# Kernel optimization log

Measured on AMD Instinct MI355X. Metric: run time of the kernel, lower is better.

## Reference

```python
import jax, jax.numpy as jnp
import numpy as np

N = 524288          # grid_size
H = 256             # MLP hidden width for psi_func
X_MIN, X_MAX = -10.0, 10.0
HBAR, MASS = 1.0, 1.0
STEPS, DT = 100, 0.01
DX = (X_MAX - X_MIN) / (N - 1)
K_TERM = -HBAR ** 2 / (2.0 * MASS)


def setup_inputs() -> dict:
    key = jax.random.key(0)
    k1, k2, k3, k4 = jax.random.split(key, 4)
    x = jnp.linspace(X_MIN, X_MAX, N, dtype=jnp.float32).reshape(-1, 1)
    V_x = (0.5 * x ** 2).astype(jnp.float32)            # harmonic potential [N,1]
    W1 = jax.random.normal(k1, (1, H), jnp.float32) * 0.5
    b1 = jax.random.normal(k2, (H,), jnp.float32) * 0.5
    W2 = jax.random.normal(k3, (H, 2), jnp.float32) / np.float32(np.sqrt(H))
    b2 = jnp.zeros((2,), jnp.float32)
    noise = jax.random.normal(k4, (STEPS,), jnp.float32)  # Langevin diffusion draws
    init_idx = 262144                                     # torch.randint(0, grid_size, (1,)).item()
    return {"x": x, "V_x": V_x, "W1": W1, "b1": b1, "W2": W2, "b2": b2,
            "noise": noise, "init_idx": init_idx}


def reference(x, V_x, W1, b1, W2, b2, noise, init_idx):
    # psi_func: 1 -> H -> 2 tanh MLP, psi = [Re, Im]
    def psi_point(xs):                    # scalar -> [2]
        h = jnp.tanh(xs * W1[0] + b1)
        return h @ W2 + b2

    xg = x[:, 0]                          # [N]
    psi = jax.vmap(psi_point)(xg)         # [N,2]

    # kinetic_energy: Laplacian d^2 psi / dx^2 via nested forward-mode derivatives
    lap = jax.vmap(jax.jacfwd(jax.jacfwd(psi_point)))(xg)   # [N,2]
    t_psi = K_TERM * lap

    # hamiltonian_operator: H psi = T psi + V(x) psi
    h_psi = t_psi + V_x * psi             # [N,2]

    # variational_energy_loss
    densities = jnp.sum(psi * h_psi, axis=1)               # [N]
    norm_densities = jnp.sum(psi ** 2, axis=1)             # [N]
    energy = (jnp.sum(densities) * DX) / (jnp.sum(norm_densities) * DX + 1e-8)

    # hamiltonian_score_matching_collapse (fused on-device scan, no per-step syncs)
    prob = norm_densities / (jnp.sum(norm_densities) * DX + 1e-8)
    log_prob = jnp.log(prob + 1e-10)
    score = jnp.zeros_like(log_prob).at[1:-1].set(
        (log_prob[2:] - log_prob[:-2]) / (2.0 * DX))

    sqrt2dt = np.float32(np.sqrt(2.0 * DT))

    def step(c_idx, z):
        s = score[c_idx]
        shift = ((s * DT + z * sqrt2dt) / DX).astype(jnp.int32)  # int() truncates toward 0
        c_idx = jnp.clip(c_idx + shift, 0, N - 1)
        return c_idx, None

    c_final, _ = jax.lax.scan(step, jnp.asarray(init_idx, jnp.int32), noise)
    x_collapsed = xg[c_final]

    return h_psi, energy, x_collapsed
```

## Files before the change

kernel.cpp:

```cpp
#include <hip/hip_runtime.h>
#include <hip/hip_bf16.h>
#include <math.h>

#define NPTS 524288
#define HDIM 256
#define NBLK (NPTS / 256)
#define STEPS 100

constexpr float DXF       = (float)(20.0 / (NPTS - 1));
constexpr float TWODXF    = (float)(2.0 * (20.0 / (NPTS - 1)));
constexpr float DTF       = 0.01f;
constexpr float SQRT2DT   = 0.14142135623730951f;
constexpr float TWO_LOG2E = 2.8853900817779268f;

typedef float v2f __attribute__((ext_vector_type(2)));

static __device__ __forceinline__ v2f vfma(v2f a, v2f b, v2f c) {
#if __has_builtin(__builtin_elementwise_fma)
    return __builtin_elementwise_fma(a, b, c);
#else
    v2f r; r.x = fmaf(a.x, b.x, c.x); r.y = fmaf(a.y, b.y, c.y); return r;
#endif
}

__global__ void qpe_prep(const float* __restrict__ W1, const float* __restrict__ b1,
                         const float* __restrict__ W2, float* __restrict__ wk)
{
    const int h = threadIdx.x;
    const float w1  = W1[h];
    const float w20 = W2[2*h];
    const float w21 = W2[2*h + 1];
    const float w1s = w1 * w1;
    wk[h]        = w1 * TWO_LOG2E;
    wk[256 + h]  = b1[h] * TWO_LOG2E;
    wk[512 + h]  = w20;
    wk[768 + h]  = w21;
    wk[1024 + h] = w20 * w1s;
    wk[1280 + h] = w21 * w1s;
}

__global__ __launch_bounds__(256) void qpe_main(
    const float* __restrict__ x,  const float* __restrict__ V,
    const float* __restrict__ wk, const float* __restrict__ b2,
    float* __restrict__ out,      float* __restrict__ lp_arr,
    float* __restrict__ pdens,    float* __restrict__ pnd)
{
    const int i = blockIdx.x * 256 + threadIdx.x;
    const float xi = x[i];
    const float Vi = V[i];

    const v2f* __restrict__ w1k2 = (const v2f*)(wk);
    const v2f* __restrict__ b1k2 = (const v2f*)(wk + 256);
    const v2f* __restrict__ w202 = (const v2f*)(wk + 512);
    const v2f* __restrict__ w212 = (const v2f*)(wk + 768);
    const v2f* __restrict__ wg02 = (const v2f*)(wk + 1024);
    const v2f* __restrict__ wg12 = (const v2f*)(wk + 1280);

    const v2f x2   = {xi, xi};
    const v2f one2 = {1.0f, 1.0f};
    const v2f m2   = {-2.0f, -2.0f};
    v2f p0 = {0.f, 0.f}, p1 = {0.f, 0.f};
    v2f a0 = {0.f, 0.f}, a1 = {0.f, 0.f};

    #pragma unroll 8
    for (int j = 0; j < HDIM / 2; ++j) {
        const v2f u = vfma(x2, w1k2[j], b1k2[j]);
        v2f e; e.x = __builtin_amdgcn_exp2f(u.x); e.y = __builtin_amdgcn_exp2f(u.y);
        const v2f dd = e + one2;
        v2f r; r.x = __builtin_amdgcn_rcpf(dd.x); r.y = __builtin_amdgcn_rcpf(dd.y);
        const v2f t  = vfma(m2, r, one2);
        const v2f o  = vfma(-t, t, one2);
        const v2f g  = t * o;
        p0 = vfma(w202[j], t, p0);
        p1 = vfma(w212[j], t, p1);
        a0 = vfma(wg02[j], g, a0);
        a1 = vfma(wg12[j], g, a1);
    }

    const float psi0 = p0.x + p0.y + b2[0];
    const float psi1 = p1.x + p1.y + b2[1];
    const float ta0  = a0.x + a0.y;
    const float ta1  = a1.x + a1.y;

    const float hp0 = fmaf(Vi, psi0, ta0);
    const float hp1 = fmaf(Vi, psi1, ta1);
    *reinterpret_cast<float2*>(&out[2*i]) = make_float2(hp0, hp1);

    const float nd = fmaf(psi0, psi0, psi1 * psi1);
    lp_arr[i] = logf(nd);

    float dens = fmaf(psi0, hp0, psi1 * hp1);
    float ndr  = nd;
    for (int off = 32; off; off >>= 1) {
        dens += __shfl_down(dens, off);
        ndr  += __shfl_down(ndr, off);
    }
    __shared__ float sd[4], sn[4];
    const int lane = threadIdx.x & 63;
    const int wid  = threadIdx.x >> 6;
    if (lane == 0) { sd[wid] = dens; sn[wid] = ndr; }
    __syncthreads();
    if (threadIdx.x == 0) {
        pdens[blockIdx.x] = sd[0] + sd[1] + sd[2] + sd[3];
        pnd[blockIdx.x]   = sn[0] + sn[1] + sn[2] + sn[3];
    }
}

__global__ __launch_bounds__(256) void qpe_tail(
    const float* __restrict__ x,     const float* __restrict__ lp,
    const float* __restrict__ pdens, const float* __restrict__ pnd,
    const float* __restrict__ noise, const int* __restrict__ init_idx,
    float* __restrict__ out,         float* __restrict__ dummy)
{
    const int tid = threadIdx.x;
    if (tid < 64) {
        if (tid == 0) {
            int c = init_idx[0];
            for (int t = 0; t < STEPS; ++t) {
                float s = 0.0f;
                if (c > 0 && c < NPTS - 1) {
                    const float lpp = lp[c + 1];
                    const float lpm = lp[c - 1];
                    s = __fdiv_rn(__fsub_rn(lpp, lpm), TWODXF);
                }
                const float a = __fadd_rn(__fmul_rn(s, DTF),
                                          __fmul_rn(noise[t], SQRT2DT));
                const int shift = (int)__fdiv_rn(a, DXF);
                c += shift;
                c = c < 0 ? 0 : (c > NPTS - 1 ? NPTS - 1 : c);
            }
            out[2 * NPTS + 1] = x[c];
        }
    } else if (tid < 128) {
        const int l = tid - 64;
        float d = 0.f, n = 0.f;
        #pragma unroll 8
        for (int k = 0; k < 32; ++k) {
            d += pdens[l + 64 * k];
            n += pnd[l + 64 * k];
        }
        for (int off = 32; off; off >>= 1) {
            d += __shfl_down(d, off);
            n += __shfl_down(n, off);
        }
        if (l == 0)
            out[2 * NPTS] = __fdiv_rn(d * DXF, fmaf(n, DXF, 1e-8f));
    } else {
        int c0 = init_idx[0];
        int start = c0 - 65536;
        if (start < 0) start = 0;
        if (start > NPTS - 131072) start = NPTS - 131072;
        start &= ~3;
        const float4* __restrict__ src = (const float4*)(lp + start);
        const int l = tid - 128;
        float acc = 0.f;
        #pragma unroll 4
        for (int k = 0; k < 256; ++k) {
            const float4 v = src[l + 128 * k];
            acc += v.x + v.y + v.z + v.w;
        }
        if (acc == 123456.789f) dummy[0] = acc;
    }
}

extern "C" void kernel_launch(void* const* d_in, const int* in_sizes, int n_in,
                              void* d_out, int out_size, void* d_ws, size_t ws_size,
                              hipStream_t stream) {
    const float* x        = (const float*)d_in[0];
    const float* V        = (const float*)d_in[1];
    const float* W1       = (const float*)d_in[2];
    const float* b1       = (const float*)d_in[3];
    const float* W2       = (const float*)d_in[4];
    const float* b2       = (const float*)d_in[5];
    const float* noise    = (const float*)d_in[6];
    const int*   init_idx = (const int*)d_in[7];

    float* out = (float*)d_out;
    float* ws  = (float*)d_ws;

    float* lp_arr = ws;
    float* pdens  = ws + NPTS;
    float* pnd    = ws + NPTS + 2048;
    float* wk     = ws + NPTS + 4096;
    float* dummy  = ws + NPTS + 4096 + 1536;

    qpe_prep<<<1, 256, 0, stream>>>(W1, b1, W2, wk);
    qpe_main<<<NBLK, 256, 0, stream>>>(x, V, wk, b2, out, lp_arr, pdens, pnd);
    qpe_tail<<<1, 256, 0, stream>>>(x, lp_arr, pdens, pnd, noise, init_idx,
                                    out, dummy);
}
```

Before: 138.2 us.

## Fuse Langevin walk into main kernel by recomputing psi on the fly

The serial 100-step collapse walk moves out of the tail kernel into an extra block of the main kernel. At each step one wavefront recomputes psi at c±1 with the MLP, instead of reading a stored log-density array. This removes the lp_arr write, the dependent global-load chain after the main pass and the dummy prefetch. The main grid also processes two points per thread with vectorized loads and stores. The walk rebuilds x from a linspace formula rather than reading the x input, and it drops the 1e-10 epsilon inside the log, which could slightly change the chosen index.

Measured after the change: 155.3 us. 12.4% more time.

```diff
diff --git a/kernel.cpp b/kernel.cpp
--- a/kernel.cpp
+++ b/kernel.cpp
@@ -4,14 +4,14 @@
 
 #define NPTS 524288
 #define HDIM 256
-#define NBLK (NPTS / 256)
+#define NBLK2 (NPTS / 512)
 #define STEPS 100
 
-constexpr float DXF       = (float)(20.0 / (NPTS - 1));
-constexpr float TWODXF    = (float)(2.0 * (20.0 / (NPTS - 1)));
-constexpr float DTF       = 0.01f;
-constexpr float SQRT2DT   = 0.14142135623730951f;
-constexpr float TWO_LOG2E = 2.8853900817779268f;
+constexpr float DXF        = (float)(20.0 / (NPTS - 1));
+constexpr float DTF        = 0.01f;
+constexpr float SQRT2DT    = 0.14142135623730951f;
+constexpr float TWO_LOG2E  = 2.8853900817779268f;
+constexpr float LN2_O_2DX  = (float)(0.6931471805599453 / (2.0 * (20.0 / (NPTS - 1))));
 
 typedef float v2f __attribute__((ext_vector_type(2)));
 
@@ -39,15 +39,87 @@
     wk[1280 + h] = w21 * w1s;
 }
 
+static __device__ void qpe_walk(const float* __restrict__ x,
+                                const float* __restrict__ wk,
+                                const float* __restrict__ b2,
+                                const float* __restrict__ noise,
+                                const int*  __restrict__ init_idx,
+                                float* __restrict__ out)
+{
+    const int lane = threadIdx.x & 63;
+    float w1r[4], b1r[4], w20r[4], w21r[4];
+    #pragma unroll
+    for (int k = 0; k < 4; ++k) {
+        const int h = lane + 64 * k;
+        w1r[k]  = wk[h];
+        b1r[k]  = wk[256 + h];
+        w20r[k] = wk[512 + h];
+        w21r[k] = wk[768 + h];
+    }
+    const float b20 = b2[0], b21 = b2[1];
+
+    int c = init_idx[0];
+    for (int t = 0; t < STEPS; ++t) {
+        const float zs = __fmul_rn(noise[t], SQRT2DT);
+        float s = 0.0f;
+        if (c > 0 && c < NPTS - 1) {
+            const float xm = fmaf((float)(c - 1), DXF, -10.0f);
+            const float xp = fmaf((float)(c + 1), DXF, -10.0f);
+            float P0m = 0.f, P1m = 0.f, P0p = 0.f, P1p = 0.f;
+            #pragma unroll
+            for (int k = 0; k < 4; ++k) {
+                const float um = fmaf(xm, w1r[k], b1r[k]);
+                const float up = fmaf(xp, w1r[k], b1r[k]);
+                const float em = __builtin_amdgcn_exp2f(um);
+                const float ep = __builtin_amdgcn_exp2f(up);
+                const float rm = __builtin_amdgcn_rcpf(em + 1.0f);
+                const float rp = __builtin_amdgcn_rcpf(ep + 1.0f);
+                const float tm = fmaf(-2.0f, rm, 1.0f);
+                const float tp = fmaf(-2.0f, rp, 1.0f);
+                P0m = fmaf(w20r[k], tm, P0m);
+                P1m = fmaf(w21r[k], tm, P1m);
+                P0p = fmaf(w20r[k], tp, P0p);
+                P1p = fmaf(w21r[k], tp, P1p);
+            }
+            #pragma unroll
+            for (int off = 32; off; off >>= 1) {
+                P0m += __shfl_xor(P0m, off);
+                P1m += __shfl_xor(P1m, off);
+                P0p += __shfl_xor(P0p, off);
+                P1p += __shfl_xor(P1p, off);
+            }
+            const float p0m = b20 + P0m, p1m = b21 + P1m;
+            const float p0p = b20 + P0p, p1p = b21 + P1p;
+            const float ndm = fmaf(p0m, p0m, p1m * p1m);
+            const float ndp = fmaf(p0p, p0p, p1p * p1p);
+            const float l2m = __builtin_amdgcn_logf(ndm);
+            const float l2p = __builtin_amdgcn_logf(ndp);
+            s = __fmul_rn(__fsub_rn(l2p, l2m), LN2_O_2DX);
+        }
+        const float a = __fadd_rn(__fmul_rn(s, DTF), zs);
+        const int shift = (int)__fdiv_rn(a, DXF);
+        c += shift;
+        c = c < 0 ? 0 : (c > NPTS - 1 ? NPTS - 1 : c);
+    }
+    if (lane == 0) out[2 * NPTS + 1] = x[c];
+}
+
 __global__ __launch_bounds__(256) void qpe_main(
     const float* __restrict__ x,  const float* __restrict__ V,
     const float* __restrict__ wk, const float* __restrict__ b2,
-    float* __restrict__ out,      float* __restrict__ lp_arr,
-    float* __restrict__ pdens,    float* __restrict__ pnd)
-{
+    float* __restrict__ out,      float* __restrict__ pdens,
+    float* __restrict__ pnd,      const float* __restrict__ noise,
+    const int* __restrict__ init_idx)
+{
+    if (blockIdx.x == NBLK2) {
+        if (threadIdx.x < 64)
+            qpe_walk(x, wk, b2, noise, init_idx, out);
+        return;
+    }
+
     const int i = blockIdx.x * 256 + threadIdx.x;
-    const float xi = x[i];
-    const float Vi = V[i];
+    const float2 xv = reinterpret_cast<const float2*>(x)[i];
+    const float2 Vv = reinterpret_cast<const float2*>(V)[i];
 
     const v2f* __restrict__ w1k2 = (const v2f*)(wk);
     const v2f* __restrict__ b1k2 = (const v2f*)(wk + 256);
@@ -56,41 +128,62 @@
     const v2f* __restrict__ wg02 = (const v2f*)(wk + 1024);
     const v2f* __restrict__ wg12 = (const v2f*)(wk + 1280);
 
-    const v2f x2   = {xi, xi};
+    const v2f xa   = {xv.x, xv.x};
+    const v2f xb   = {xv.y, xv.y};
     const v2f one2 = {1.0f, 1.0f};
     const v2f m2   = {-2.0f, -2.0f};
-    v2f p0 = {0.f, 0.f}, p1 = {0.f, 0.f};
-    v2f a0 = {0.f, 0.f}, a1 = {0.f, 0.f};
-
-    #pragma unroll 8
+    v2f pa0 = {0.f,0.f}, pa1 = {0.f,0.f}, aa0 = {0.f,0.f}, aa1 = {0.f,0.f};
+    v2f pb0 = {0.f,0.f}, pb1 = {0.f,0.f}, ab0 = {0.f,0.f}, ab1 = {0.f,0.f};
+
+    #pragma unroll 4
     for (int j = 0; j < HDIM / 2; ++j) {
-        const v2f u = vfma(x2, w1k2[j], b1k2[j]);
-        v2f e; e.x = __builtin_amdgcn_exp2f(u.x); e.y = __builtin_amdgcn_exp2f(u.y);
-        const v2f dd = e + one2;
-        v2f r; r.x = __builtin_amdgcn_rcpf(dd.x); r.y = __builtin_amdgcn_rcpf(dd.y);
-        const v2f t  = vfma(m2, r, one2);
-        const v2f o  = vfma(-t, t, one2);
-        const v2f g  = t * o;
-        p0 = vfma(w202[j], t, p0);
-        p1 = vfma(w212[j], t, p1);
-        a0 = vfma(wg02[j], g, a0);
-        a1 = vfma(wg12[j], g, a1);
-    }
-
-    const float psi0 = p0.x + p0.y + b2[0];
-    const float psi1 = p1.x + p1.y + b2[1];
-    const float ta0  = a0.x + a0.y;
-    const float ta1  = a1.x + a1.y;
-
-    const float hp0 = fmaf(Vi, psi0, ta0);
-    const float hp1 = fmaf(Vi, psi1, ta1);
-    *reinterpret_cast<float2*>(&out[2*i]) = make_float2(hp0, hp1);
-
-    const float nd = fmaf(psi0, psi0, psi1 * psi1);
-    lp_arr[i] = logf(nd);
-
-    float dens = fmaf(psi0, hp0, psi1 * hp1);
-    float ndr  = nd;
+        const v2f w1 = w1k2[j];
+        const v2f bb = b1k2[j];
+        const v2f ua = vfma(xa, w1, bb);
+        const v2f ub = vfma(xb, w1, bb);
+        v2f ea, eb;
+        ea.x = __builtin_amdgcn_exp2f(ua.x); ea.y = __builtin_amdgcn_exp2f(ua.y);
+        eb.x = __builtin_amdgcn_exp2f(ub.x); eb.y = __builtin_amdgcn_exp2f(ub.y);
+        const v2f da = ea + one2;
+        const v2f db = eb + one2;
+        v2f ra, rb;
+        ra.x = __builtin_amdgcn_rcpf(da.x); ra.y = __builtin_amdgcn_rcpf(da.y);
+        rb.x = __builtin_amdgcn_rcpf(db.x); rb.y = __builtin_amdgcn_rcpf(db.y);
+        const v2f ta = vfma(m2, ra, one2);
+        const v2f tb = vfma(m2, rb, one2);
+        const v2f oa = vfma(-ta, ta, one2);
+        const v2f ob = vfma(-tb, tb, one2);
+        const v2f ga = ta * oa;
+        const v2f gb = tb * ob;
+        const v2f w20 = w202[j], w21 = w212[j];
+        const v2f g0  = wg02[j], g1  = wg12[j];
+        pa0 = vfma(w20, ta, pa0);  pa1 = vfma(w21, ta, pa1);
+        aa0 = vfma(g0,  ga, aa0);  aa1 = vfma(g1,  ga, aa1);
+        pb0 = vfma(w20, tb, pb0);  pb1 = vfma(w21, tb, pb1);
+        ab0 = vfma(g0,  gb, ab0);  ab1 = vfma(g1,  gb, ab1);
+    }
+
+    const float b20 = b2[0], b21 = b2[1];
+    const float psiA0 = pa0.x + pa0.y + b20;
+    const float psiA1 = pa1.x + pa1.y + b21;
+    const float psiB0 = pb0.x + pb0.y + b20;
+    const float psiB1 = pb1.x + pb1.y + b21;
+    const float taA0 = aa0.x + aa0.y, taA1 = aa1.x + aa1.y;
+    const float taB0 = ab0.x + ab0.y, taB1 = ab1.x + ab1.y;
+
+    const float hpA0 = fmaf(Vv.x, psiA0, taA0);
+    const float hpA1 = fmaf(Vv.x, psiA1, taA1);
+    const float hpB0 = fmaf(Vv.y, psiB0, taB0);
+    const float hpB1 = fmaf(Vv.y, psiB1, taB1);
+    float4 o4; o4.x = hpA0; o4.y = hpA1; o4.z = hpB0; o4.w = hpB1;
+    reinterpret_cast<float4*>(out)[i] = o4;
+
+    const float ndA = fmaf(psiA0, psiA0, psiA1 * psiA1);
+    const float ndB = fmaf(psiB0, psiB0, psiB1 * psiB1);
+    float dens = fmaf(psiA0, hpA0, psiA1 * hpA1) + fmaf(psiB0, hpB0, psiB1 * hpB1);
+    float ndr  = ndA + ndB;
+
+    #pragma unroll
     for (int off = 32; off; off >>= 1) {
         dens += __shfl_down(dens, off);
         ndr  += __shfl_down(ndr, off);
@@ -106,60 +199,27 @@
     }
 }
 
-__global__ __launch_bounds__(256) void qpe_tail(
-    const float* __restrict__ x,     const float* __restrict__ lp,
+__global__ __launch_bounds__(256) void qpe_reduce(
     const float* __restrict__ pdens, const float* __restrict__ pnd,
-    const float* __restrict__ noise, const int* __restrict__ init_idx,
-    float* __restrict__ out,         float* __restrict__ dummy)
+    float* __restrict__ energy_out)
 {
     const int tid = threadIdx.x;
-    if (tid < 64) {
-        if (tid == 0) {
-            int c = init_idx[0];
-            for (int t = 0; t < STEPS; ++t) {
-                float s = 0.0f;
-                if (c > 0 && c < NPTS - 1) {
-                    const float lpp = lp[c + 1];
-                    const float lpm = lp[c - 1];
-                    s = __fdiv_rn(__fsub_rn(lpp, lpm), TWODXF);
-                }
-                const float a = __fadd_rn(__fmul_rn(s, DTF),
-                                          __fmul_rn(noise[t], SQRT2DT));
-                const int shift = (int)__fdiv_rn(a, DXF);
-                c += shift;
-                c = c < 0 ? 0 : (c > NPTS - 1 ? NPTS - 1 : c);
-            }
-            out[2 * NPTS + 1] = x[c];
-        }
-    } else if (tid < 128) {
-        const int l = tid - 64;
-        float d = 0.f, n = 0.f;
-        #pragma unroll 8
-        for (int k = 0; k < 32; ++k) {
-            d += pdens[l + 64 * k];
-            n += pnd[l + 64 * k];
-        }
-        for (int off = 32; off; off >>= 1) {
-            d += __shfl_down(d, off);
-            n += __shfl_down(n, off);
-        }
-        if (l == 0)
-            out[2 * NPTS] = __fdiv_rn(d * DXF, fmaf(n, DXF, 1e-8f));
-    } else {
-        int c0 = init_idx[0];
-        int start = c0 - 65536;
-        if (start < 0) start = 0;
-        if (start > NPTS - 131072) start = NPTS - 131072;
-        start &= ~3;
-        const float4* __restrict__ src = (const float4*)(lp + start);
-        const int l = tid - 128;
-        float acc = 0.f;
-        #pragma unroll 4
-        for (int k = 0; k < 256; ++k) {
-            const float4 v = src[l + 128 * k];
-            acc += v.x + v.y + v.z + v.w;
-        }
-        if (acc == 123456.789f) dummy[0] = acc;
+    float d = pdens[tid] + pdens[tid + 256] + pdens[tid + 512] + pdens[tid + 768];
+    float n = pnd[tid]   + pnd[tid + 256]   + pnd[tid + 512]   + pnd[tid + 768];
+    #pragma unroll
+    for (int off = 32; off; off >>= 1) {
+        d += __shfl_down(d, off);
+        n += __shfl_down(n, off);
+    }
+    __shared__ float sd[4], sn[4];
+    const int lane = tid & 63;
+    const int wid  = tid >> 6;
+    if (lane == 0) { sd[wid] = d; sn[wid] = n; }
+    __syncthreads();
+    if (tid == 0) {
+        const float Sd = sd[0] + sd[1] + sd[2] + sd[3];
+        const float Sn = sn[0] + sn[1] + sn[2] + sn[3];
+        energy_out[0] = __fdiv_rn(Sd * DXF, fmaf(Sn, DXF, 1e-8f));
     }
 }
 
@@ -178,14 +238,12 @@
     float* out = (float*)d_out;
     float* ws  = (float*)d_ws;
 
-    float* lp_arr = ws;
-    float* pdens  = ws + NPTS;
-    float* pnd    = ws + NPTS + 2048;
-    float* wk     = ws + NPTS + 4096;
-    float* dummy  = ws + NPTS + 4096 + 1536;
+    float* wk    = ws;
+    float* pdens = ws + 2048;
+    float* pnd   = ws + 4096;
 
     qpe_prep<<<1, 256, 0, stream>>>(W1, b1, W2, wk);
-    qpe_main<<<NBLK, 256, 0, stream>>>(x, V, wk, b2, out, lp_arr, pdens, pnd);
-    qpe_tail<<<1, 256, 0, stream>>>(x, lp_arr, pdens, pnd, noise, init_idx,
-                                    out, dummy);
-}
+    qpe_main<<<NBLK2 + 1, 256, 0, stream>>>(x, V, wk, b2, out, pdens, pnd,
+                                            noise, init_idx);
+    qpe_reduce<<<1, 256, 0, stream>>>(pdens, pnd, out + 2 * NPTS);
+}
```
